# Optimization experiments

Hardware: AMD Instinct MI355X
Metric: run time of the kernel (lower is better)

The kernel has to match this reference:

```python
import jax, jax.numpy as jnp
import numpy as np

D_MODEL = 1024
H = 16
D_HEAD = D_MODEL // H  # 64


def setup_inputs() -> dict:
    key = jax.random.key(0)
    ks = jax.random.split(key, 11)
    B, L = 4, 1024
    s = 0.02
    return {
        "Q": jax.random.normal(ks[0], (B, L, D_MODEL), jnp.float32),
        "K": jax.random.normal(ks[1], (B, L, D_MODEL), jnp.float32),
        "V": jax.random.normal(ks[2], (B, L, D_MODEL), jnp.float32),
        # per-head Dense weights stacked on a leading head axis (Keras Dense: y = x @ W + b)
        "Wq": jax.random.normal(ks[3], (H, D_MODEL, D_HEAD), jnp.float32) * s,
        "bq": jnp.zeros((H, D_HEAD), jnp.float32),
        "Wk": jax.random.normal(ks[4], (H, D_MODEL, D_HEAD), jnp.float32) * s,
        "bk": jnp.zeros((H, D_HEAD), jnp.float32),
        "Wv": jax.random.normal(ks[5], (H, D_MODEL, D_HEAD), jnp.float32) * s,
        "bv": jnp.zeros((H, D_HEAD), jnp.float32),
        "Wo": jax.random.normal(ks[6], (D_MODEL, D_MODEL), jnp.float32) * s,
        "bo": jnp.zeros((D_MODEL,), jnp.float32),
    }


def reference(Q, K, V, Wq, bq, Wk, bk, Wv, bv, Wo, bo):
    # per-head projections, vectorized over heads: [B, H, L, Dh]
    q = jnp.einsum("bld,hde->bhle", Q, Wq) + bq[None, :, None, :]
    k = jnp.einsum("bld,hde->bhle", K, Wk) + bk[None, :, None, :]
    v = jnp.einsum("bld,hde->bhle", V, Wv) + bv[None, :, None, :]
    # scaled dot-product attention scores: [B, H, Lq, Lk]
    scores = jnp.einsum("bhqe,bhke->bhqk", q, k) / jnp.sqrt(jnp.asarray(D_HEAD, q.dtype))
    attn = jax.nn.softmax(scores, axis=-1)
    out_h = jnp.einsum("bhqk,bhke->bhqe", attn, v)  # [B, H, Lq, Dh]
    # concat heads along feature dim (matches tf.concat(heads, axis=2))
    B, Hh, Lq, Dh = out_h.shape
    concat = out_h.transpose(0, 2, 1, 3).reshape(B, Lq, Hh * Dh)
    output = concat @ Wo + bo
    # tf.stack(heads_attention) -> [H, B, Lq, Lk]
    attention = attn.transpose(1, 0, 2, 3)
    return output, attention
```

## Files before the change

kernel.cpp:

```cpp
#include <hip/hip_runtime.h>
#include <stdint.h>

#define DEVI __device__ __forceinline__
typedef unsigned short u16;
typedef __attribute__((ext_vector_type(8))) short s16x8;
typedef __attribute__((ext_vector_type(4))) float f32x4;

typedef __attribute__((address_space(1))) void as1_void;
typedef __attribute__((address_space(3))) void as3_void;

DEVI u16 f2b(float f){
  union { float f; uint32_t u; } x; x.f = f;
  return (u16)((x.u + 0x7fffu + ((x.u >> 16) & 1u)) >> 16);
}
DEVI float b2f(u16 u){
  union { uint32_t u; float f; } x; x.u = ((uint32_t)u) << 16;
  return x.f;
}
DEVI void gload16(const void* g, void* l){
  __builtin_amdgcn_global_load_lds((as1_void*)g, (as3_void*)l, 16, 0, 0);
}
DEVI f32x4 MFMA(s16x8 a, s16x8 b, f32x4 c){
  return __builtin_amdgcn_mfma_f32_16x16x32_bf16(a, b, c, 0, 0, 0);
}

__global__ __launch_bounds__(256)
void k_prep(const float* __restrict__ Q, const float* __restrict__ Kc,
            const float* __restrict__ V,
            u16* __restrict__ Qb, u16* __restrict__ Kb, u16* __restrict__ Vb,
            const float* __restrict__ Wq, const float* __restrict__ Wk,
            const float* __restrict__ Wv, const float* __restrict__ Wo,
            u16* __restrict__ WqT, u16* __restrict__ WkT,
            u16* __restrict__ WvT, u16* __restrict__ WoT){
  __shared__ float t[64][65];
  const int bid = blockIdx.x, tid = threadIdx.x;
  if(bid < 12288){
    int tno = bid >> 12;
    int blk = bid & 4095;
    const float* s = (tno == 0) ? Q : (tno == 1) ? Kc : V;
    u16* d = (tno == 0) ? Qb : (tno == 1) ? Kb : Vb;
    int i = (blk * 256 + tid) * 4;
    float4 v = *(const float4*)(s + i);
    ushort4 o;
    o.x = f2b(v.x); o.y = f2b(v.y); o.z = f2b(v.z); o.w = f2b(v.w);
    *(ushort4*)(d + i) = o;
  } else {
    int j = bid - 12288;
    const float* src; u16* dst; int C, r0, c0;
    if(j < 768){
      int tno = j >> 8, rem = j & 255, head = rem >> 4, rt = rem & 15;
      src = ((tno == 0) ? Wq : (tno == 1) ? Wk : Wv) + head * 65536;
      dst = ((tno == 0) ? WqT : (tno == 1) ? WkT : WvT) + head * 65536;
      C = 64; r0 = rt * 64; c0 = 0;
    } else {
      int j2 = j - 768;
      src = Wo; dst = WoT; C = 1024;
      r0 = (j2 & 15) * 64; c0 = (j2 >> 4) * 64;
    }
    int tx = tid & 63, ty = tid >> 6;
    #pragma unroll
    for(int i2 = 0; i2 < 64; i2 += 4)
      t[ty + i2][tx] = src[(size_t)(r0 + ty + i2) * C + c0 + tx];
    __syncthreads();
    #pragma unroll
    for(int i2 = 0; i2 < 64; i2 += 4)
      dst[(size_t)(c0 + ty + i2) * 1024 + r0 + tx] = f2b(t[tx][ty + i2]);
  }
}

template<int BM, int BK>
DEVI void gemm_core(int mode, const u16* __restrict__ A, const u16* __restrict__ Bt,
                    const float* __restrict__ bias, void* __restrict__ Cp,
                    int m0, int n0, u16* sAb, u16* sBb){
  const int tid = threadIdx.x, w = tid >> 6, l = tid & 63;
  const int wr = w >> 1, wc = w & 1;
  constexpr int MI = BM / 32;
  constexpr int KK = BK / 32;
  constexpr int CPR = BK / 8;
  constexpr int CPT_A = BM * BK / 2048;
  constexpr int CPT_B = 128 * BK / 2048;
  constexpr int RB = 2 * BK;
  f32x4 acc[MI][4];
  #pragma unroll
  for(int a = 0; a < MI; a++)
    #pragma unroll
    for(int b = 0; b < 4; b++) acc[a][b] = (f32x4){0.f, 0.f, 0.f, 0.f};

  const int NT = 1024 / BK;
  auto STAGE = [&](int buf, int t){
    #pragma unroll
    for(int s2 = 0; s2 < CPT_A; s2++){
      int c = s2 * 256 + tid;
      int r = c / CPR, ch = (c % CPR) ^ (r & (CPR - 1));
      gload16((const char*)A + ((size_t)(m0 + r) * 1024 + t * BK) * 2 + ch * 16,
              (char*)sAb + (size_t)buf * BM * RB + c * 16);
    }
    #pragma unroll
    for(int s2 = 0; s2 < CPT_B; s2++){
      int c = s2 * 256 + tid;
      int r = c / CPR, ch = (c % CPR) ^ (r & (CPR - 1));
      gload16((const char*)Bt + ((size_t)(n0 + r) * 1024 + t * BK) * 2 + ch * 16,
              (char*)sBb + (size_t)buf * 128 * RB + c * 16);
    }
  };
  STAGE(0, 0);
  __syncthreads();
  for(int t = 0; t < NT; t++){
    const int cur = t & 1;
    if(t + 1 < NT) STAGE(cur ^ 1, t + 1);
    const char* pa = (const char*)sAb + (size_t)cur * BM * RB;
    const char* pb = (const char*)sBb + (size_t)cur * 128 * RB;
    s16x8 af[MI][KK], bf[4][KK];
    #pragma unroll
    for(int mi = 0; mi < MI; mi++){
      int r = (BM / 2) * wr + 16 * mi + (l & 15);
      #pragma unroll
      for(int kk = 0; kk < KK; kk++)
        af[mi][kk] = *(const s16x8*)(pa + r * RB +
                     ((kk * 64 + 16 * (l >> 4)) ^ ((r & (CPR - 1)) << 4)));
    }
    #pragma unroll
    for(int ni = 0; ni < 4; ni++){
      int r = 64 * wc + 16 * ni + (l & 15);
      #pragma unroll
      for(int kk = 0; kk < KK; kk++)
        bf[ni][kk] = *(const s16x8*)(pb + r * RB +
                     ((kk * 64 + 16 * (l >> 4)) ^ ((r & (CPR - 1)) << 4)));
    }
    #pragma unroll
    for(int kk = 0; kk < KK; kk++)
      #pragma unroll
      for(int mi = 0; mi < MI; mi++)
        #pragma unroll
        for(int ni = 0; ni < 4; ni++)
          acc[mi][ni] = MFMA(af[mi][kk], bf[ni][kk], acc[mi][ni]);
    __syncthreads();
  }
  #pragma unroll
  for(int mi = 0; mi < MI; mi++){
    #pragma unroll
    for(int ni = 0; ni < 4; ni++){
      #pragma unroll
      for(int i = 0; i < 4; i++){
        int gr = m0 + (BM / 2) * wr + 16 * mi + 4 * (l >> 4) + i;
        int gc = n0 + 64 * wc + 16 * ni + (l & 15);
        float v = acc[mi][ni][i];
        if(mode == 0){
          ((u16*)Cp)[(size_t)gr * 1024 + gc] = f2b(v + bias[gc]);
        } else if(mode == 1){
          ((u16*)Cp)[((size_t)(gc >> 10) << 20) + ((size_t)gr << 10) + (gc & 1023)] =
              f2b(v + bias[gr]);
        } else {
          ((float*)Cp)[(size_t)gr * 1024 + gc] = v + bias[gc];
        }
      }
    }
  }
}

__global__ __launch_bounds__(256, 3)
void k_proj(const u16* __restrict__ Qb, const u16* __restrict__ Kb,
            const u16* __restrict__ Vb,
            const u16* __restrict__ WqT, const u16* __restrict__ WkT,
            const u16* __restrict__ WvT,
            const float* __restrict__ bq, const float* __restrict__ bk,
            const float* __restrict__ bv,
            u16* __restrict__ q_ws, u16* __restrict__ k_ws, u16* __restrict__ vT_ws){
  __shared__ u16 sA[2][128 * 32];
  __shared__ u16 sB[2][128 * 32];
  const int raw = blockIdx.x;
  const int bid = (raw & 7) * 96 + (raw >> 3);
  if(bid < 256){
    gemm_core<128, 32>(0, Qb, WqT, bq, q_ws, (bid >> 3) * 128, (bid & 7) * 128,
                       &sA[0][0], &sB[0][0]);
  } else if(bid < 512){
    int b2 = bid - 256;
    gemm_core<128, 32>(0, Kb, WkT, bk, k_ws, (b2 >> 3) * 128, (b2 & 7) * 128,
                       &sA[0][0], &sB[0][0]);
  } else {
    int b2 = bid - 512;
    gemm_core<128, 32>(1, WvT, Vb, bv, vT_ws, (b2 >> 5) * 128, (b2 & 31) * 128,
                       &sA[0][0], &sB[0][0]);
  }
}

__global__ __launch_bounds__(256)
void k_final(const u16* __restrict__ A, const u16* __restrict__ Bt,
             const float* __restrict__ bias, float* __restrict__ C){
  __shared__ u16 sA[2][64 * 64];
  __shared__ u16 sB[2][128 * 64];
  const int raw = blockIdx.x;
  const int bid = (raw & 7) * 64 + (raw >> 3);
  gemm_core<64, 64>(2, A, Bt, bias, C, (bid >> 3) * 64, (bid & 7) * 128,
                    &sA[0][0], &sB[0][0]);
}

__global__ __launch_bounds__(512, 2)
void k_attn(const u16* __restrict__ qws, const u16* __restrict__ kws,
            const u16* __restrict__ vws, float* __restrict__ attn,
            u16* __restrict__ concat){
  __shared__ u16 k_s[2][64 * 64];
  __shared__ u16 v_s[2][64 * 64];
  __shared__ u16 p_s[128 * 64];
  const int tid = threadIdx.x, w = tid >> 6, l = tid & 63;
  const int bx = blockIdx.x;
  const int bh = bx & 63, qb = bx >> 6, b = bh >> 4, h = bh & 15;
  const char* qg = (const char*)qws + ((size_t)(b * 1024 + qb * 128) * 1024 + h * 64) * 2;
  const char* kg = (const char*)kws + ((size_t)(b * 1024) * 1024 + h * 64) * 2;
  const char* vg = (const char*)vws + ((size_t)b * 1048576 + (size_t)h * 64 * 1024) * 2;
  float* ao = attn + (size_t)((h * 4 + b) * 1024 + qb * 128) * 1024;
  u16* cw = concat + (size_t)(b * 1024 + qb * 128) * 1024 + h * 64;

  auto STAGEK = [&](int buf, int kt){
    int r = tid >> 3, ch = tid & 7;
    gload16(kg + (size_t)(kt * 64 + r) * 2048 + ((ch ^ (r & 7)) * 16),
            (char*)k_s[buf] + tid * 16);
  };
  auto STAGEV = [&](int buf, int kt){
    int e = tid >> 3, ch = tid & 7;
    gload16(vg + (size_t)e * 2048 + kt * 128 + ((ch ^ (e & 7)) * 16),
            (char*)v_s[buf] + tid * 16);
  };

  s16x8 af0, af1;
  {
    int rq = 16 * w + (l & 15);
    af0 = *(const s16x8*)(qg + (size_t)rq * 2048 + (l >> 4) * 16);
    af1 = *(const s16x8*)(qg + (size_t)rq * 2048 + 64 + (l >> 4) * 16);
  }

  const float KS = 0.18033688011112042f;
  float rs[4] = {0.f, 0.f, 0.f, 0.f};

  STAGEK(0, 0);
  __syncthreads();
  for(int kt = 0; kt < 16; kt++){
    const int cur = kt & 1;
    if(kt + 1 < 16) STAGEK(cur ^ 1, kt + 1);
    #pragma unroll
    for(int f = 0; f < 4; f++){
      int r = 16 * f + (l & 15);
      s16x8 b0 = *(const s16x8*)((const char*)k_s[cur] + r * 128 + ((16 * (l >> 4)) ^ ((r & 7) << 4)));
      s16x8 b1 = *(const s16x8*)((const char*)k_s[cur] + r * 128 + ((64 + 16 * (l >> 4)) ^ ((r & 7) << 4)));
      f32x4 sf = (f32x4){0.f, 0.f, 0.f, 0.f};
      sf = MFMA(af0, b0, sf);
      sf = MFMA(af1, b1, sf);
      #pragma unroll
      for(int i = 0; i < 4; i++) rs[i] += exp2f(sf[i] * KS);
    }
    __syncthreads();
  }
  #pragma unroll
  for(int i = 0; i < 4; i++){
    #pragma unroll
    for(int m = 1; m < 16; m <<= 1) rs[i] += __shfl_xor(rs[i], m, 64);
  }
  float inv[4];
  #pragma unroll
  for(int i = 0; i < 4; i++) inv[i] = 1.0f / rs[i];

  f32x4 oacc[4];
  #pragma unroll
  for(int fe = 0; fe < 4; fe++) oacc[fe] = (f32x4){0.f, 0.f, 0.f, 0.f};

  STAGEK(0, 0);
  STAGEV(0, 0);
  __syncthreads();
  for(int kt = 0; kt < 16; kt++){
    const int cur = kt & 1;
    if(kt + 1 < 16){ STAGEK(cur ^ 1, kt + 1); STAGEV(cur ^ 1, kt + 1); }
    f32x4 sf[4];
    #pragma unroll
    for(int f = 0; f < 4; f++){
      int r = 16 * f + (l & 15);
      s16x8 b0 = *(const s16x8*)((const char*)k_s[cur] + r * 128 + ((16 * (l >> 4)) ^ ((r & 7) << 4)));
      s16x8 b1 = *(const s16x8*)((const char*)k_s[cur] + r * 128 + ((64 + 16 * (l >> 4)) ^ ((r & 7) << 4)));
      sf[f] = (f32x4){0.f, 0.f, 0.f, 0.f};
      sf[f] = MFMA(af0, b0, sf[f]);
      sf[f] = MFMA(af1, b1, sf[f]);
    }
    #pragma unroll
    for(int f = 0; f < 4; f++){
      #pragma unroll
      for(int i = 0; i < 4; i++){
        float p = exp2f(sf[f][i] * KS) * inv[i];
        int rr = 16 * w + 4 * (l >> 4) + i;
        int cc = 16 * f + (l & 15);
        *(u16*)((char*)p_s + rr * 128 + ((cc * 2) ^ ((rr & 7) << 4))) = f2b(p);
      }
    }
    #pragma unroll
    for(int kc = 0; kc < 2; kc++){
      int rp = 16 * w + (l & 15);
      s16x8 pa = *(const s16x8*)((const char*)p_s + rp * 128 +
                  ((kc * 64 + 16 * (l >> 4)) ^ ((rp & 7) << 4)));
      #pragma unroll
      for(int fe = 0; fe < 4; fe++){
        int e = 16 * fe + (l & 15);
        s16x8 bv = *(const s16x8*)((const char*)v_s[cur] + e * 128 +
                    ((kc * 64 + 16 * (l >> 4)) ^ ((e & 7) << 4)));
        oacc[fe] = MFMA(pa, bv, oacc[fe]);
      }
    }
    #pragma unroll
    for(int it = 0; it < 4; it++){
      int row = 16 * w + 4 * it + (l >> 4);
      uint2 pv = *(const uint2*)((const char*)p_s + row * 128 +
                                 ((8 * (l & 15)) ^ ((row & 7) << 4)));
      f32x4 o;
      o[0] = b2f((u16)(pv.x & 0xffffu));
      o[1] = b2f((u16)(pv.x >> 16));
      o[2] = b2f((u16)(pv.y & 0xffffu));
      o[3] = b2f((u16)(pv.y >> 16));
      *(f32x4*)(ao + (size_t)row * 1024 + kt * 64 + (l & 15) * 4) = o;
    }
    __syncthreads();
  }
  #pragma unroll
  for(int fe = 0; fe < 4; fe++){
    #pragma unroll
    for(int i = 0; i < 4; i++){
      int qi = 16 * w + 4 * (l >> 4) + i;
      cw[(size_t)qi * 1024 + 16 * fe + (l & 15)] = f2b(oacc[fe][i]);
    }
  }
}

extern "C" void kernel_launch(void* const* d_in, const int* in_sizes, int n_in,
                              void* d_out, int out_size, void* d_ws, size_t ws_size,
                              hipStream_t stream){
  const float* Q  = (const float*)d_in[0];
  const float* Kc = (const float*)d_in[1];
  const float* V  = (const float*)d_in[2];
  const float* Wq = (const float*)d_in[3];
  const float* bq = (const float*)d_in[4];
  const float* Wk = (const float*)d_in[5];
  const float* bk = (const float*)d_in[6];
  const float* Wv = (const float*)d_in[7];
  const float* bv = (const float*)d_in[8];
  const float* Wo = (const float*)d_in[9];
  const float* bo = (const float*)d_in[10];
  float* out = (float*)d_out;

  char* ws = (char*)d_ws;
  u16* q_ws      = (u16*)(ws + 0);
  u16* k_ws      = (u16*)(ws + 8388608);
  u16* vT_ws     = (u16*)(ws + 16777216);
  u16* concat_ws = (u16*)(ws + 25165824);
  u16* WqT = (u16*)(ws + 33554432);
  u16* WkT = (u16*)(ws + 35651584);
  u16* WvT = (u16*)(ws + 37748736);
  u16* WoT = (u16*)(ws + 39845888);

  u16* Qb = (u16*)((char*)d_out + 16777216);
  u16* Kb = (u16*)((char*)d_out + 25165824);
  u16* Vb = (u16*)((char*)d_out + 33554432);
  float* attn = out + 4194304;

  k_prep<<<13312, 256, 0, stream>>>(Q, Kc, V, Qb, Kb, Vb,
                                    Wq, Wk, Wv, Wo, WqT, WkT, WvT, WoT);
  k_proj<<<768, 256, 0, stream>>>(Qb, Kb, Vb, WqT, WkT, WvT, bq, bk, bv,
                                  q_ws, k_ws, vT_ws);
  k_attn<<<512, 512, 0, stream>>>(q_ws, k_ws, vT_ws, attn, concat_ws);
  k_final<<<512, 256, 0, stream>>>(concat_ws, WoT, bo, out);
}
```

Measured before the change: 158.3 us.

## Triple-buffer K/V tiles in attention with prefetch distance two and explicit vmcnt waits

Both attention passes (the row-sum pass and the P·V pass) now use three LDS buffers for K and V tiles instead of two. Tiles are prefetched two iterations ahead. The `__syncthreads` calls are replaced by explicit `s_waitcnt vmcnt(N)` plus `s_barrier`, so the code waits only for the tile it is about to use. The aim is to hide global-to-LDS load latency behind MFMA work. In exchange, LDS use per block rises to 64 KB, which may constrain occupancy. The hand-counted vmcnt values must also match the interleaved attn stores, or the kernel reads stale data.

```diff
diff --git a/kernel.cpp b/kernel.cpp
--- a/kernel.cpp
+++ b/kernel.cpp
@@ -199,8 +199,8 @@
 void k_attn(const u16* __restrict__ qws, const u16* __restrict__ kws,
             const u16* __restrict__ vws, float* __restrict__ attn,
             u16* __restrict__ concat){
-  __shared__ u16 k_s[2][64 * 64];
-  __shared__ u16 v_s[2][64 * 64];
+  __shared__ u16 k_s[3][64 * 64];
+  __shared__ u16 v_s[3][64 * 64];
   __shared__ u16 p_s[128 * 64];
   const int tid = threadIdx.x, w = tid >> 6, l = tid & 63;
   const int bx = blockIdx.x;
@@ -233,22 +233,39 @@
   float rs[4] = {0.f, 0.f, 0.f, 0.f};
 
   STAGEK(0, 0);
-  __syncthreads();
-  for(int kt = 0; kt < 16; kt++){
-    const int cur = kt & 1;
-    if(kt + 1 < 16) STAGEK(cur ^ 1, kt + 1);
-    #pragma unroll
-    for(int f = 0; f < 4; f++){
-      int r = 16 * f + (l & 15);
-      s16x8 b0 = *(const s16x8*)((const char*)k_s[cur] + r * 128 + ((16 * (l >> 4)) ^ ((r & 7) << 4)));
-      s16x8 b1 = *(const s16x8*)((const char*)k_s[cur] + r * 128 + ((64 + 16 * (l >> 4)) ^ ((r & 7) << 4)));
-      f32x4 sf = (f32x4){0.f, 0.f, 0.f, 0.f};
-      sf = MFMA(af0, b0, sf);
-      sf = MFMA(af1, b1, sf);
-      #pragma unroll
-      for(int i = 0; i < 4; i++) rs[i] += exp2f(sf[i] * KS);
-    }
-    __syncthreads();
+  STAGEK(1, 1);
+  __builtin_amdgcn_sched_barrier(0);
+  asm volatile("s_waitcnt vmcnt(1) lgkmcnt(0)" ::: "memory");
+  __builtin_amdgcn_s_barrier();
+  __builtin_amdgcn_sched_barrier(0);
+  {
+    int cur = 0;
+    for(int kt = 0; kt < 16; kt++){
+      if(kt + 2 < 16){
+        int pre = cur + 2; if(pre >= 3) pre -= 3;
+        STAGEK(pre, kt + 2);
+      }
+      __builtin_amdgcn_sched_barrier(0);
+      #pragma unroll
+      for(int f = 0; f < 4; f++){
+        int r = 16 * f + (l & 15);
+        s16x8 b0 = *(const s16x8*)((const char*)k_s[cur] + r * 128 + ((16 * (l >> 4)) ^ ((r & 7) << 4)));
+        s16x8 b1 = *(const s16x8*)((const char*)k_s[cur] + r * 128 + ((64 + 16 * (l >> 4)) ^ ((r & 7) << 4)));
+        f32x4 sf = (f32x4){0.f, 0.f, 0.f, 0.f};
+        sf = MFMA(af0, b0, sf);
+        sf = MFMA(af1, b1, sf);
+        #pragma unroll
+        for(int i = 0; i < 4; i++) rs[i] += exp2f(sf[i] * KS);
+      }
+      if(kt < 15){
+        __builtin_amdgcn_sched_barrier(0);
+        if(kt <= 13) asm volatile("s_waitcnt vmcnt(1) lgkmcnt(0)" ::: "memory");
+        else         asm volatile("s_waitcnt vmcnt(0) lgkmcnt(0)" ::: "memory");
+        __builtin_amdgcn_s_barrier();
+        __builtin_amdgcn_sched_barrier(0);
+      }
+      cur = (cur == 2) ? 0 : cur + 1;
+    }
   }
   #pragma unroll
   for(int i = 0; i < 4; i++){
@@ -259,62 +276,84 @@
   #pragma unroll
   for(int i = 0; i < 4; i++) inv[i] = 1.0f / rs[i];
 
+  asm volatile("s_waitcnt lgkmcnt(0)" ::: "memory");
+  __builtin_amdgcn_s_barrier();
+  __builtin_amdgcn_sched_barrier(0);
+
   f32x4 oacc[4];
   #pragma unroll
   for(int fe = 0; fe < 4; fe++) oacc[fe] = (f32x4){0.f, 0.f, 0.f, 0.f};
 
-  STAGEK(0, 0);
-  STAGEV(0, 0);
-  __syncthreads();
-  for(int kt = 0; kt < 16; kt++){
-    const int cur = kt & 1;
-    if(kt + 1 < 16){ STAGEK(cur ^ 1, kt + 1); STAGEV(cur ^ 1, kt + 1); }
-    f32x4 sf[4];
-    #pragma unroll
-    for(int f = 0; f < 4; f++){
-      int r = 16 * f + (l & 15);
-      s16x8 b0 = *(const s16x8*)((const char*)k_s[cur] + r * 128 + ((16 * (l >> 4)) ^ ((r & 7) << 4)));
-      s16x8 b1 = *(const s16x8*)((const char*)k_s[cur] + r * 128 + ((64 + 16 * (l >> 4)) ^ ((r & 7) << 4)));
-      sf[f] = (f32x4){0.f, 0.f, 0.f, 0.f};
-      sf[f] = MFMA(af0, b0, sf[f]);
-      sf[f] = MFMA(af1, b1, sf[f]);
-    }
-    #pragma unroll
-    for(int f = 0; f < 4; f++){
-      #pragma unroll
-      for(int i = 0; i < 4; i++){
-        float p = exp2f(sf[f][i] * KS) * inv[i];
-        int rr = 16 * w + 4 * (l >> 4) + i;
-        int cc = 16 * f + (l & 15);
-        *(u16*)((char*)p_s + rr * 128 + ((cc * 2) ^ ((rr & 7) << 4))) = f2b(p);
-      }
-    }
-    #pragma unroll
-    for(int kc = 0; kc < 2; kc++){
-      int rp = 16 * w + (l & 15);
-      s16x8 pa = *(const s16x8*)((const char*)p_s + rp * 128 +
-                  ((kc * 64 + 16 * (l >> 4)) ^ ((rp & 7) << 4)));
-      #pragma unroll
-      for(int fe = 0; fe < 4; fe++){
-        int e = 16 * fe + (l & 15);
-        s16x8 bv = *(const s16x8*)((const char*)v_s[cur] + e * 128 +
-                    ((kc * 64 + 16 * (l >> 4)) ^ ((e & 7) << 4)));
-        oacc[fe] = MFMA(pa, bv, oacc[fe]);
-      }
-    }
-    #pragma unroll
-    for(int it = 0; it < 4; it++){
-      int row = 16 * w + 4 * it + (l >> 4);
-      uint2 pv = *(const uint2*)((const char*)p_s + row * 128 +
-                                 ((8 * (l & 15)) ^ ((row & 7) << 4)));
-      f32x4 o;
-      o[0] = b2f((u16)(pv.x & 0xffffu));
-      o[1] = b2f((u16)(pv.x >> 16));
-      o[2] = b2f((u16)(pv.y & 0xffffu));
-      o[3] = b2f((u16)(pv.y >> 16));
-      *(f32x4*)(ao + (size_t)row * 1024 + kt * 64 + (l & 15) * 4) = o;
-    }
-    __syncthreads();
+  STAGEK(0, 0); STAGEV(0, 0);
+  STAGEK(1, 1); STAGEV(1, 1);
+  __builtin_amdgcn_sched_barrier(0);
+  asm volatile("s_waitcnt vmcnt(2) lgkmcnt(0)" ::: "memory");
+  __builtin_amdgcn_s_barrier();
+  __builtin_amdgcn_sched_barrier(0);
+  {
+    int cur = 0;
+    for(int kt = 0; kt < 16; kt++){
+      if(kt + 2 < 16){
+        int pre = cur + 2; if(pre >= 3) pre -= 3;
+        STAGEK(pre, kt + 2);
+        STAGEV(pre, kt + 2);
+      }
+      __builtin_amdgcn_sched_barrier(0);
+      f32x4 sf[4];
+      #pragma unroll
+      for(int f = 0; f < 4; f++){
+        int r = 16 * f + (l & 15);
+        s16x8 b0 = *(const s16x8*)((const char*)k_s[cur] + r * 128 + ((16 * (l >> 4)) ^ ((r & 7) << 4)));
+        s16x8 b1 = *(const s16x8*)((const char*)k_s[cur] + r * 128 + ((64 + 16 * (l >> 4)) ^ ((r & 7) << 4)));
+        sf[f] = (f32x4){0.f, 0.f, 0.f, 0.f};
+        sf[f] = MFMA(af0, b0, sf[f]);
+        sf[f] = MFMA(af1, b1, sf[f]);
+      }
+      #pragma unroll
+      for(int f = 0; f < 4; f++){
+        #pragma unroll
+        for(int i = 0; i < 4; i++){
+          float p = exp2f(sf[f][i] * KS) * inv[i];
+          int rr = 16 * w + 4 * (l >> 4) + i;
+          int cc = 16 * f + (l & 15);
+          *(u16*)((char*)p_s + rr * 128 + ((cc * 2) ^ ((rr & 7) << 4))) = f2b(p);
+        }
+      }
+      #pragma unroll
+      for(int kc = 0; kc < 2; kc++){
+        int rp = 16 * w + (l & 15);
+        s16x8 pa = *(const s16x8*)((const char*)p_s + rp * 128 +
+                    ((kc * 64 + 16 * (l >> 4)) ^ ((rp & 7) << 4)));
+        #pragma unroll
+        for(int fe = 0; fe < 4; fe++){
+          int e = 16 * fe + (l & 15);
+          s16x8 bv = *(const s16x8*)((const char*)v_s[cur] + e * 128 +
+                      ((kc * 64 + 16 * (l >> 4)) ^ ((e & 7) << 4)));
+          oacc[fe] = MFMA(pa, bv, oacc[fe]);
+        }
+      }
+      #pragma unroll
+      for(int it = 0; it < 4; it++){
+        int row = 16 * w + 4 * it + (l >> 4);
+        uint2 pv = *(const uint2*)((const char*)p_s + row * 128 +
+                                   ((8 * (l & 15)) ^ ((row & 7) << 4)));
+        f32x4 o;
+        o[0] = b2f((u16)(pv.x & 0xffffu));
+        o[1] = b2f((u16)(pv.x >> 16));
+        o[2] = b2f((u16)(pv.y & 0xffffu));
+        o[3] = b2f((u16)(pv.y >> 16));
+        *(f32x4*)(ao + (size_t)row * 1024 + kt * 64 + (l & 15) * 4) = o;
+      }
+      if(kt < 15){
+        __builtin_amdgcn_sched_barrier(0);
+        if(kt == 0)       asm volatile("s_waitcnt vmcnt(6) lgkmcnt(0)" ::: "memory");
+        else if(kt <= 13) asm volatile("s_waitcnt vmcnt(10) lgkmcnt(0)" ::: "memory");
+        else              asm volatile("s_waitcnt vmcnt(8) lgkmcnt(0)" ::: "memory");
+        __builtin_amdgcn_s_barrier();
+        __builtin_amdgcn_sched_barrier(0);
+      }
+      cur = (cur == 2) ? 0 : cur + 1;
+    }
   }
   #pragma unroll
   for(int fe = 0; fe < 4; fe++){
```

Measured after the change: 158.7 us. Within noise of the previous version (+0.3%).
